# Kernel tuning notes

Hardware: AMD Instinct MI355X
Metric: run time of the kernel (lower is better)

## Reference

```python
import jax, jax.numpy as jnp
import numpy as np

EPS = 1e-5

def _bn_eval(x, gamma, beta, mu, var):
    # channelwise BN (eval mode) on [B,C,N,K]
    inv = gamma / jnp.sqrt(var + EPS)
    return x * inv[None, :, None, None] + (beta - mu * inv)[None, :, None, None]

def _gather_nk(x, idx):
    # x: [B,C,N], idx: [B,N,K] -> [B,C,N,K]
    return jnp.take_along_axis(x[:, :, None, :], idx[:, None, :, :], axis=3)

def setup_inputs() -> dict:
    key = jax.random.key(0)
    ks = jax.random.split(key, 20)
    B, N, K, C = 2, 16384, 16, 128
    s = 0.05
    inp = {
        'coord': jax.random.normal(ks[0], (B, N, 3), jnp.float32),
        'feature_spa': jax.random.normal(ks[1], (B, C, N), jnp.float32),
        'feature_spe': jax.random.normal(ks[2], (B, C, N), jnp.float32),
        'neighbor_indices': jax.random.randint(ks[3], (B, N, K), 0, N),
        'wq': jax.random.normal(ks[4], (C, C), jnp.float32) * s,
        'wk': jax.random.normal(ks[5], (C, C), jnp.float32) * s,
        'wv_w': jax.random.normal(ks[6], (C, C), jnp.float32) * s,
        'wv_b': jax.random.normal(ks[7], (C,), jnp.float32) * s,
        'pos_w1': jax.random.normal(ks[8], (3, 3), jnp.float32) * 0.3,
        'pos_b1': jax.random.normal(ks[9], (3,), jnp.float32) * 0.1,
        'pos_g': jnp.ones((3,), jnp.float32),
        'pos_beta': jnp.zeros((3,), jnp.float32),
        'pos_mu': jnp.zeros((3,), jnp.float32),
        'pos_var': jnp.ones((3,), jnp.float32),
        'pos_w2': jax.random.normal(ks[10], (1, 3), jnp.float32) * 0.3,
        'pos_b2': jax.random.normal(ks[11], (1,), jnp.float32) * 0.1,
        'sc_w1': jax.random.normal(ks[12], (2, 2), jnp.float32) * 0.3,
        'sc_b1': jax.random.normal(ks[13], (2,), jnp.float32) * 0.1,
        'sc_g': jnp.ones((2,), jnp.float32),
        'sc_beta': jnp.zeros((2,), jnp.float32),
        'sc_mu': jnp.zeros((2,), jnp.float32),
        'sc_var': jnp.ones((2,), jnp.float32),
        'sc_w2': jax.random.normal(ks[14], (1, 2), jnp.float32) * 0.3,
        'sc_b2': jax.random.normal(ks[15], (1,), jnp.float32) * 0.1,
    }
    return inp

def reference(coord, feature_spa, feature_spe, neighbor_indices,
              wq, wk, wv_w, wv_b,
              pos_w1, pos_b1, pos_g, pos_beta, pos_mu, pos_var, pos_w2, pos_b2,
              sc_w1, sc_b1, sc_g, sc_beta, sc_mu, sc_var, sc_w2, sc_b2):
    C = feature_spa.shape[1]
    coord_t = jnp.transpose(coord, (0, 2, 1))                      # [B,3,N]
    Q = jnp.einsum('oc,bcn->bon', wq, feature_spa)                 # [B,C,N]
    Kf = jnp.einsum('oc,bcn->bon', wk, feature_spe)
    V = jnp.einsum('oc,bcn->bon', wv_w, feature_spe) + wv_b[None, :, None]
    # positional branch
    neighbor_coord = _gather_nk(coord_t, neighbor_indices)         # [B,3,N,K]
    coord_diff = neighbor_coord - coord_t[:, :, :, None]
    g = jnp.exp(-2.0 * coord_diff ** 2)                            # [B,3,N,K]
    h = jnp.einsum('oc,bcnk->bonk', pos_w1, g) + pos_b1[None, :, None, None]
    h = jax.nn.relu(_bn_eval(h, pos_g, pos_beta, pos_mu, pos_var))
    scores_coord = jnp.einsum('oc,bcnk->bonk', pos_w2, h) + pos_b2[None, :, None, None]  # [B,1,N,K]
    # feature branch
    Kg = _gather_nk(Kf, neighbor_indices)                          # [B,C,N,K]
    Vg = _gather_nk(V, neighbor_indices)                           # [B,C,N,K]
    scores_feat = jnp.einsum('bcn,bcnk->bnk', Q, Kg) / np.sqrt(C)  # [B,N,K]
    scores = jnp.concatenate([scores_coord, scores_feat[:, None]], axis=1)  # [B,2,N,K]
    s = jnp.einsum('oc,bcnk->bonk', sc_w1, scores) + sc_b1[None, :, None, None]
    s = jax.nn.relu(_bn_eval(s, sc_g, sc_beta, sc_mu, sc_var))
    s = jnp.einsum('oc,bcnk->bonk', sc_w2, s) + sc_b2[None, :, None, None]  # [B,1,N,K]
    attn = jax.nn.softmax(s, axis=-1)                              # [B,1,N,K]
    fusion_feat = jnp.sum(attn * Vg, axis=-1)                      # [B,C,N]
    return fusion_feat
```

## Files before the change

### kernel.cpp

```cpp
#include <hip/hip_runtime.h>
#include <cstdint>
#include <cstddef>

#define B_ 2
#define N_ 16384
#define K_ 16
#define C_ 128

typedef __attribute__((ext_vector_type(8))) short  bf16x8;
typedef __attribute__((ext_vector_type(4))) float  f32x4;

__device__ __forceinline__ float bfu_lo(uint32_t w) { return __uint_as_float(w << 16); }
__device__ __forceinline__ float bfu_hi(uint32_t w) { return __uint_as_float(w & 0xffff0000u); }

__device__ __forceinline__ ushort f32_to_bf16_rne(float x) {
    uint32_t u = __float_as_uint(x);
    u += 0x7FFFu + ((u >> 16) & 1u);
    return (ushort)(u >> 16);
}

__device__ __forceinline__ int xswz(int n, int c) {
    return n * 128 + ((((c >> 3) ^ (n & 7)) << 3) | (c & 7));
}

__global__ __launch_bounds__(256) void qkv_gemm(
    const float* __restrict__ spa, const float* __restrict__ spe,
    const float* __restrict__ wq, const float* __restrict__ wk,
    const float* __restrict__ wv, const float* __restrict__ wvb,
    ushort* __restrict__ Qt16, ushort* __restrict__ Kt16, ushort* __restrict__ Vt16)
{
    const int nt    = blockIdx.x * 64;
    const int b     = blockIdx.y;
    const int which = blockIdx.z;
    const float* X = (which == 0) ? spa : spe;
    const float* W = (which == 0) ? wq : (which == 1 ? wk : wv);
    ushort* Out    = (which == 0) ? Qt16 : (which == 1 ? Kt16 : Vt16);

    __shared__ ushort xs[64 * 128];

    const int t    = threadIdx.x;
    const int w    = t >> 6;
    const int lane = t & 63;
    const int l15  = lane & 15;
    const int l4   = lane >> 4;
    const int ow   = (w & 1) * 64;
    const int nw   = (w >> 1) * 32;

    {
        const int c  = t >> 1;
        const int nh = (t & 1) * 32;
        const float* xrow = X + ((size_t)b * C_ + c) * N_ + nt + nh;
        #pragma unroll
        for (int q = 0; q < 8; ++q) {
            float4 v = ((const float4*)xrow)[q];
            const int n = nh + q * 4;
            xs[xswz(n + 0, c)] = f32_to_bf16_rne(v.x);
            xs[xswz(n + 1, c)] = f32_to_bf16_rne(v.y);
            xs[xswz(n + 2, c)] = f32_to_bf16_rne(v.z);
            xs[xswz(n + 3, c)] = f32_to_bf16_rne(v.w);
        }
    }
    __syncthreads();

    f32x4 acc[4][2];
    #pragma unroll
    for (int of = 0; of < 4; ++of)
        #pragma unroll
        for (int nf = 0; nf < 2; ++nf)
            acc[of][nf] = (f32x4){0.f, 0.f, 0.f, 0.f};

    #pragma unroll
    for (int kc = 0; kc < 4; ++kc) {
        const int cb = kc * 32 + l4 * 8;
        bf16x8 afr[4];
        #pragma unroll
        for (int of = 0; of < 4; ++of) {
            const int row = ow + of * 16 + l15;
            const float* wp = W + (size_t)row * C_ + cb;
            float4 wa = *(const float4*)wp;
            float4 wb = *(const float4*)(wp + 4);
            afr[of][0] = (short)f32_to_bf16_rne(wa.x);
            afr[of][1] = (short)f32_to_bf16_rne(wa.y);
            afr[of][2] = (short)f32_to_bf16_rne(wa.z);
            afr[of][3] = (short)f32_to_bf16_rne(wa.w);
            afr[of][4] = (short)f32_to_bf16_rne(wb.x);
            afr[of][5] = (short)f32_to_bf16_rne(wb.y);
            afr[of][6] = (short)f32_to_bf16_rne(wb.z);
            afr[of][7] = (short)f32_to_bf16_rne(wb.w);
        }
        bf16x8 bfr[2];
        #pragma unroll
        for (int nf = 0; nf < 2; ++nf) {
            const int n = nw + nf * 16 + l15;
            bfr[nf] = *(__shared__ bf16x8*)&xs[xswz(n, kc * 32 + l4 * 8)];
        }
        #pragma unroll
        for (int of = 0; of < 4; ++of)
            #pragma unroll
            for (int nf = 0; nf < 2; ++nf)
                acc[of][nf] = __builtin_amdgcn_mfma_f32_16x16x32_bf16(
                    afr[of], bfr[nf], acc[of][nf], 0, 0, 0);
    }

    #pragma unroll
    for (int of = 0; of < 4; ++of) {
        const int o0r = ow + of * 16 + l4 * 4;
        float4 bv = make_float4(0.f, 0.f, 0.f, 0.f);
        if (which == 2) bv = *(const float4*)(wvb + o0r);
        #pragma unroll
        for (int nf = 0; nf < 2; ++nf) {
            const int n = nt + nw + nf * 16 + l15;
            uint2 pk;
            pk.x = (uint32_t)f32_to_bf16_rne(acc[of][nf][0] + bv.x)
                 | ((uint32_t)f32_to_bf16_rne(acc[of][nf][1] + bv.y) << 16);
            pk.y = (uint32_t)f32_to_bf16_rne(acc[of][nf][2] + bv.z)
                 | ((uint32_t)f32_to_bf16_rne(acc[of][nf][3] + bv.w) << 16);
            *(uint2*)(Out + ((size_t)b * N_ + n) * C_ + o0r) = pk;
        }
    }
}

__global__ __launch_bounds__(256) void attn_fuse(
    const float* __restrict__ coord, const int* __restrict__ nbr,
    const ushort* __restrict__ Qt16, const ushort* __restrict__ Kt16,
    const ushort* __restrict__ Vt16,
    const float* __restrict__ pw1, const float* __restrict__ pb1,
    const float* __restrict__ pg,  const float* __restrict__ pbeta,
    const float* __restrict__ pmu, const float* __restrict__ pvar,
    const float* __restrict__ pw2, const float* __restrict__ pb2,
    const float* __restrict__ sw1, const float* __restrict__ sb1,
    const float* __restrict__ sg,  const float* __restrict__ sbeta,
    const float* __restrict__ smu, const float* __restrict__ svar,
    const float* __restrict__ sw2, const float* __restrict__ sb2,
    float* __restrict__ out)
{
    const int bid  = blockIdx.x;
    const int b    = bid >> 10;
    const int n0   = (bid & 1023) << 4;
    const int t    = threadIdx.x;
    const int w    = t >> 6;
    const int lane = t & 63;
    const int g    = lane >> 2;
    const int sub  = lane & 3;

    __shared__ float qs[16][132];
    __shared__ int   idx_s[16][16];
    __shared__ float cs[16][3];
    __shared__ float ot[128][17];

    {
        const int n = t >> 4, c0 = (t & 15) * 8;
        uint4 qw = *(const uint4*)(Qt16 + ((size_t)(b * N_ + n0 + n)) * C_ + c0);
        qs[n][c0 + 0] = bfu_lo(qw.x); qs[n][c0 + 1] = bfu_hi(qw.x);
        qs[n][c0 + 2] = bfu_lo(qw.y); qs[n][c0 + 3] = bfu_hi(qw.y);
        qs[n][c0 + 4] = bfu_lo(qw.z); qs[n][c0 + 5] = bfu_hi(qw.z);
        qs[n][c0 + 6] = bfu_lo(qw.w); qs[n][c0 + 7] = bfu_hi(qw.w);
        idx_s[t >> 4][t & 15] = nbr[((size_t)(b * N_ + n0 + (t >> 4))) * K_ + (t & 15)];
        if (t < 48) cs[t / 3][t % 3] = coord[((size_t)(b * N_ + n0 + t / 3)) * 3 + (t % 3)];
    }
    __syncthreads();

    float pinv[3], pofs[3], w1r[3][3], w2r[3], pb1r[3];
    #pragma unroll
    for (int o = 0; o < 3; ++o) {
        float inv = pg[o] / sqrtf(pvar[o] + 1e-5f);
        pinv[o] = inv;
        pofs[o] = pbeta[o] - pmu[o] * inv;
        pb1r[o] = pb1[o];
        w2r[o]  = pw2[o];
        #pragma unroll
        for (int i2 = 0; i2 < 3; ++i2) w1r[o][i2] = pw1[o * 3 + i2];
    }
    const float pb2v = pb2[0];
    float sinv[2], sofs[2], sb1r[2];
    #pragma unroll
    for (int o = 0; o < 2; ++o) {
        float inv = sg[o] / sqrtf(svar[o] + 1e-5f);
        sinv[o] = inv;
        sofs[o] = sbeta[o] - smu[o] * inv;
        sb1r[o] = sb1[o];
    }
    const float sw1r[4] = {sw1[0], sw1[1], sw1[2], sw1[3]};
    const float sw2r[2] = {sw2[0], sw2[1]};
    const float sb2v = sb2[0];
    const float inv_sqrtC = 0.088388347648318447f;

    #pragma unroll
    for (int i = 0; i < 4; ++i) {
        const int nl = w * 4 + i;
        const int idxg = idx_s[nl][g];

        const uint4* kp = (const uint4*)(Kt16 + ((size_t)(b * N_ + idxg)) * C_ + sub * 32);
        uint4 kw0 = kp[0], kw1 = kp[1], kw2 = kp[2], kw3 = kp[3];
        uint32_t vv[16];
        #pragma unroll
        for (int k = 0; k < 16; ++k) {
            const int vid = idx_s[nl][k];
            vv[k] = ((const uint32_t*)(Vt16 + ((size_t)(b * N_ + vid)) * C_))[lane];
        }
        const float* ncp = coord + ((size_t)(b * N_ + idxg)) * 3;
        const float nc0 = ncp[0], nc1 = ncp[1], nc2 = ncp[2];

        const float* qrow = &qs[nl][sub * 32];
        float acc = 0.f;
        #pragma unroll
        for (int j = 0; j < 4; ++j) {
            float4 qa = *(const float4*)&qrow[j * 8];
            float4 qb = *(const float4*)&qrow[j * 8 + 4];
            uint4  kwj = (j == 0) ? kw0 : (j == 1) ? kw1 : (j == 2) ? kw2 : kw3;
            acc = fmaf(qa.x, bfu_lo(kwj.x), acc);
            acc = fmaf(qa.y, bfu_hi(kwj.x), acc);
            acc = fmaf(qa.z, bfu_lo(kwj.y), acc);
            acc = fmaf(qa.w, bfu_hi(kwj.y), acc);
            acc = fmaf(qb.x, bfu_lo(kwj.z), acc);
            acc = fmaf(qb.y, bfu_hi(kwj.z), acc);
            acc = fmaf(qb.z, bfu_lo(kwj.w), acc);
            acc = fmaf(qb.w, bfu_hi(kwj.w), acc);
        }
        acc += __shfl_xor(acc, 1);
        acc += __shfl_xor(acc, 2);
        const float sfeat = acc * inv_sqrtC;

        float d0 = nc0 - cs[nl][0], d1 = nc1 - cs[nl][1], d2 = nc2 - cs[nl][2];
        float g0 = expf(-2.f * d0 * d0);
        float g1 = expf(-2.f * d1 * d1);
        float g2 = expf(-2.f * d2 * d2);
        float h0 = fmaf(w1r[0][0], g0, fmaf(w1r[0][1], g1, fmaf(w1r[0][2], g2, pb1r[0])));
        float h1 = fmaf(w1r[1][0], g0, fmaf(w1r[1][1], g1, fmaf(w1r[1][2], g2, pb1r[1])));
        float h2 = fmaf(w1r[2][0], g0, fmaf(w1r[2][1], g1, fmaf(w1r[2][2], g2, pb1r[2])));
        h0 = fmaxf(fmaf(h0, pinv[0], pofs[0]), 0.f);
        h1 = fmaxf(fmaf(h1, pinv[1], pofs[1]), 0.f);
        h2 = fmaxf(fmaf(h2, pinv[2], pofs[2]), 0.f);
        const float scoord = fmaf(w2r[0], h0, fmaf(w2r[1], h1, fmaf(w2r[2], h2, pb2v)));

        float t0 = fmaf(sw1r[0], scoord, fmaf(sw1r[1], sfeat, sb1r[0]));
        t0 = fmaxf(fmaf(t0, sinv[0], sofs[0]), 0.f);
        float t1 = fmaf(sw1r[2], scoord, fmaf(sw1r[3], sfeat, sb1r[1]));
        t1 = fmaxf(fmaf(t1, sinv[1], sofs[1]), 0.f);
        float s = fmaf(sw2r[0], t0, fmaf(sw2r[1], t1, sb2v));

        float m = s;
        m = fmaxf(m, __shfl_xor(m, 4));
        m = fmaxf(m, __shfl_xor(m, 8));
        m = fmaxf(m, __shfl_xor(m, 16));
        m = fmaxf(m, __shfl_xor(m, 32));
        float e = expf(s - m);
        float den = e;
        den += __shfl_xor(den, 4);
        den += __shfl_xor(den, 8);
        den += __shfl_xor(den, 16);
        den += __shfl_xor(den, 32);
        const float attn = e / den;

        float a0 = 0.f, a1 = 0.f;
        #pragma unroll
        for (int k = 0; k < 16; ++k) {
            const float ak = __shfl(attn, k << 2);
            a0 = fmaf(ak, bfu_lo(vv[k]), a0);
            a1 = fmaf(ak, bfu_hi(vv[k]), a1);
        }
        ot[2 * lane][nl]     = a0;
        ot[2 * lane + 1][nl] = a1;
    }
    __syncthreads();

    {
        const int col = t & 15;
        const int r0  = (t >> 4) * 8;
        #pragma unroll
        for (int r = 0; r < 8; ++r)
            out[((size_t)(b * C_ + r0 + r)) * N_ + n0 + col] = ot[r0 + r][col];
    }
}

extern "C" void kernel_launch(void* const* d_in, const int* in_sizes, int n_in,
                              void* d_out, int out_size, void* d_ws, size_t ws_size,
                              hipStream_t stream) {
    const float* coord = (const float*)d_in[0];
    const float* spa   = (const float*)d_in[1];
    const float* spe   = (const float*)d_in[2];
    const int*   nbr   = (const int*)  d_in[3];
    const float* wq    = (const float*)d_in[4];
    const float* wk    = (const float*)d_in[5];
    const float* wv    = (const float*)d_in[6];
    const float* wvb   = (const float*)d_in[7];
    const float* pw1   = (const float*)d_in[8];
    const float* pb1   = (const float*)d_in[9];
    const float* pg    = (const float*)d_in[10];
    const float* pbeta = (const float*)d_in[11];
    const float* pmu   = (const float*)d_in[12];
    const float* pvar  = (const float*)d_in[13];
    const float* pw2   = (const float*)d_in[14];
    const float* pb2   = (const float*)d_in[15];
    const float* sw1   = (const float*)d_in[16];
    const float* sb1   = (const float*)d_in[17];
    const float* sg    = (const float*)d_in[18];
    const float* sbeta = (const float*)d_in[19];
    const float* smu   = (const float*)d_in[20];
    const float* svar  = (const float*)d_in[21];
    const float* sw2   = (const float*)d_in[22];
    const float* sb2   = (const float*)d_in[23];
    float* out = (float*)d_out;

    ushort* Qt16 = (ushort*)d_ws;
    ushort* Kt16 = Qt16 + (size_t)B_ * N_ * C_;
    ushort* Vt16 = Kt16 + (size_t)B_ * N_ * C_;

    qkv_gemm<<<dim3(N_ / 64, B_, 3), 256, 0, stream>>>(
        spa, spe, wq, wk, wv, wvb, Qt16, Kt16, Vt16);

    attn_fuse<<<dim3(B_ * N_ / 16), 256, 0, stream>>>(
        coord, nbr, Qt16, Kt16, Vt16,
        pw1, pb1, pg, pbeta, pmu, pvar, pw2, pb2,
        sw1, sb1, sg, sbeta, smu, svar, sw2, sb2,
        out);
}
```

Measured before the change: 192.3 us.

## Pre-convert QKV weights to bf16 and stage them in LDS with larger GEMM tiles

Adds a small kernel that converts the three weight matrices to bf16 once per call. The QKV GEMM then loads the whole bf16 weight matrix into swizzled shared memory instead of reading and converting fp32 weights from global memory in every block. The N tile grows from 64 to 128 with 512 threads, which halves the number of blocks and raises reuse. In exchange it adds a kernel launch, needs 64KB of LDS per block (which may limit occupancy), and uses extra workspace for the converted weights.

```diff
diff --git a/kernel.cpp b/kernel.cpp
--- a/kernel.cpp
+++ b/kernel.cpp
@@ -18,42 +18,72 @@
     u += 0x7FFFu + ((u >> 16) & 1u);
     return (ushort)(u >> 16);
 }
-
-__device__ __forceinline__ int xswz(int n, int c) {
-    return n * 128 + ((((c >> 3) ^ (n & 7)) << 3) | (c & 7));
-}
-
-__global__ __launch_bounds__(256) void qkv_gemm(
+__device__ __forceinline__ uint32_t pack_bf16x2(float lo, float hi) {
+    return (uint32_t)f32_to_bf16_rne(lo) | ((uint32_t)f32_to_bf16_rne(hi) << 16);
+}
+
+__device__ __forceinline__ int xswz(int row, int c) {
+    return row * 128 + ((((c >> 3) ^ (row & 7)) << 3) | (c & 7));
+}
+
+__global__ __launch_bounds__(256) void w_cvt(
+    const float* __restrict__ wq, const float* __restrict__ wk,
+    const float* __restrict__ wv, ushort* __restrict__ W16all)
+{
+    const float* src = (blockIdx.y == 0) ? wq : (blockIdx.y == 1 ? wk : wv);
+    ushort* dst = W16all + (size_t)blockIdx.y * (C_ * C_);
+    const int i = (blockIdx.x * 256 + threadIdx.x) * 8;
+    float4 a = *(const float4*)(src + i);
+    float4 b4 = *(const float4*)(src + i + 4);
+    uint4 pk;
+    pk.x = pack_bf16x2(a.x, a.y);
+    pk.y = pack_bf16x2(a.z, a.w);
+    pk.z = pack_bf16x2(b4.x, b4.y);
+    pk.w = pack_bf16x2(b4.z, b4.w);
+    *(uint4*)(dst + i) = pk;
+}
+
+__global__ __launch_bounds__(512) void qkv_gemm(
     const float* __restrict__ spa, const float* __restrict__ spe,
-    const float* __restrict__ wq, const float* __restrict__ wk,
-    const float* __restrict__ wv, const float* __restrict__ wvb,
+    const ushort* __restrict__ W16all, const float* __restrict__ wvb,
     ushort* __restrict__ Qt16, ushort* __restrict__ Kt16, ushort* __restrict__ Vt16)
 {
-    const int nt    = blockIdx.x * 64;
+    const int nt    = blockIdx.x * 128;
     const int b     = blockIdx.y;
     const int which = blockIdx.z;
-    const float* X = (which == 0) ? spa : spe;
-    const float* W = (which == 0) ? wq : (which == 1 ? wk : wv);
-    ushort* Out    = (which == 0) ? Qt16 : (which == 1 ? Kt16 : Vt16);
-
-    __shared__ ushort xs[64 * 128];
+    const float*  X   = (which == 0) ? spa : spe;
+    const ushort* W16 = W16all + (size_t)which * (C_ * C_);
+    ushort* Out       = (which == 0) ? Qt16 : (which == 1 ? Kt16 : Vt16);
+
+    __shared__ ushort xs[128 * 128];
+    __shared__ ushort ws[128 * 128];
 
     const int t    = threadIdx.x;
     const int w    = t >> 6;
     const int lane = t & 63;
     const int l15  = lane & 15;
     const int l4   = lane >> 4;
-    const int ow   = (w & 1) * 64;
-    const int nw   = (w >> 1) * 32;
+    const int ow   = (w & 3) * 32;
+    const int nw   = (w >> 2) * 64;
 
     {
-        const int c  = t >> 1;
-        const int nh = (t & 1) * 32;
-        const float* xrow = X + ((size_t)b * C_ + c) * N_ + nt + nh;
+        const int r  = t >> 2;
+        const int c0 = (t & 3) * 32;
+        const uint4* src = (const uint4*)(W16 + r * C_ + c0);
+        #pragma unroll
+        for (int q = 0; q < 4; ++q) {
+            uint4 v = src[q];
+            *(uint4*)&ws[xswz(r, c0 + q * 8)] = v;
+        }
+    }
+    {
+        const int c  = t >> 2;
+        const int nq = (t & 3) * 32;
+        const float* xrow = X + ((size_t)b * C_ + c) * N_ + nt + nq;
         #pragma unroll
         for (int q = 0; q < 8; ++q) {
             float4 v = ((const float4*)xrow)[q];
-            const int n = nh + q * 4;
+            const int n = nq + q * 4;
             xs[xswz(n + 0, c)] = f32_to_bf16_rne(v.x);
             xs[xswz(n + 1, c)] = f32_to_bf16_rne(v.y);
             xs[xswz(n + 2, c)] = f32_to_bf16_rne(v.z);
@@ -62,59 +92,43 @@
     }
     __syncthreads();
 
-    f32x4 acc[4][2];
-    #pragma unroll
-    for (int of = 0; of < 4; ++of)
-        #pragma unroll
-        for (int nf = 0; nf < 2; ++nf)
+    f32x4 acc[2][4];
+    #pragma unroll
+    for (int of = 0; of < 2; ++of)
+        #pragma unroll
+        for (int nf = 0; nf < 4; ++nf)
             acc[of][nf] = (f32x4){0.f, 0.f, 0.f, 0.f};
 
     #pragma unroll
     for (int kc = 0; kc < 4; ++kc) {
         const int cb = kc * 32 + l4 * 8;
-        bf16x8 afr[4];
-        #pragma unroll
-        for (int of = 0; of < 4; ++of) {
-            const int row = ow + of * 16 + l15;
-            const float* wp = W + (size_t)row * C_ + cb;
-            float4 wa = *(const float4*)wp;
-            float4 wb = *(const float4*)(wp + 4);
-            afr[of][0] = (short)f32_to_bf16_rne(wa.x);
-            afr[of][1] = (short)f32_to_bf16_rne(wa.y);
-            afr[of][2] = (short)f32_to_bf16_rne(wa.z);
-            afr[of][3] = (short)f32_to_bf16_rne(wa.w);
-            afr[of][4] = (short)f32_to_bf16_rne(wb.x);
-            afr[of][5] = (short)f32_to_bf16_rne(wb.y);
-            afr[of][6] = (short)f32_to_bf16_rne(wb.z);
-            afr[of][7] = (short)f32_to_bf16_rne(wb.w);
-        }
-        bf16x8 bfr[2];
-        #pragma unroll
-        for (int nf = 0; nf < 2; ++nf) {
-            const int n = nw + nf * 16 + l15;
-            bfr[nf] = *(__shared__ bf16x8*)&xs[xswz(n, kc * 32 + l4 * 8)];
-        }
-        #pragma unroll
-        for (int of = 0; of < 4; ++of)
+        bf16x8 afr[2];
+        #pragma unroll
+        for (int of = 0; of < 2; ++of)
+            afr[of] = *(__shared__ bf16x8*)&ws[xswz(ow + of * 16 + l15, cb)];
+        bf16x8 bfr[4];
+        #pragma unroll
+        for (int nf = 0; nf < 4; ++nf)
+            bfr[nf] = *(__shared__ bf16x8*)&xs[xswz(nw + nf * 16 + l15, cb)];
+        #pragma unroll
+        for (int of = 0; of < 2; ++of)
             #pragma unroll
-            for (int nf = 0; nf < 2; ++nf)
+            for (int nf = 0; nf < 4; ++nf)
                 acc[of][nf] = __builtin_amdgcn_mfma_f32_16x16x32_bf16(
                     afr[of], bfr[nf], acc[of][nf], 0, 0, 0);
     }
 
     #pragma unroll
-    for (int of = 0; of < 4; ++of) {
+    for (int of = 0; of < 2; ++of) {
         const int o0r = ow + of * 16 + l4 * 4;
         float4 bv = make_float4(0.f, 0.f, 0.f, 0.f);
         if (which == 2) bv = *(const float4*)(wvb + o0r);
         #pragma unroll
-        for (int nf = 0; nf < 2; ++nf) {
+        for (int nf = 0; nf < 4; ++nf) {
             const int n = nt + nw + nf * 16 + l15;
             uint2 pk;
-            pk.x = (uint32_t)f32_to_bf16_rne(acc[of][nf][0] + bv.x)
-                 | ((uint32_t)f32_to_bf16_rne(acc[of][nf][1] + bv.y) << 16);
-            pk.y = (uint32_t)f32_to_bf16_rne(acc[of][nf][2] + bv.z)
-                 | ((uint32_t)f32_to_bf16_rne(acc[of][nf][3] + bv.w) << 16);
+            pk.x = pack_bf16x2(acc[of][nf][0] + bv.x, acc[of][nf][1] + bv.y);
+            pk.y = pack_bf16x2(acc[of][nf][2] + bv.z, acc[of][nf][3] + bv.w);
             *(uint2*)(Out + ((size_t)b * N_ + n) * C_ + o0r) = pk;
         }
     }
@@ -302,12 +316,15 @@
     const float* sb2   = (const float*)d_in[23];
     float* out = (float*)d_out;
 
-    ushort* Qt16 = (ushort*)d_ws;
-    ushort* Kt16 = Qt16 + (size_t)B_ * N_ * C_;
-    ushort* Vt16 = Kt16 + (size_t)B_ * N_ * C_;
-
-    qkv_gemm<<<dim3(N_ / 64, B_, 3), 256, 0, stream>>>(
-        spa, spe, wq, wk, wv, wvb, Qt16, Kt16, Vt16);
+    ushort* Qt16  = (ushort*)d_ws;
+    ushort* Kt16  = Qt16 + (size_t)B_ * N_ * C_;
+    ushort* Vt16  = Kt16 + (size_t)B_ * N_ * C_;
+    ushort* W16all = Vt16 + (size_t)B_ * N_ * C_;
+
+    w_cvt<<<dim3(8, 3), 256, 0, stream>>>(wq, wk, wv, W16all);
+
+    qkv_gemm<<<dim3(N_ / 128, B_, 3), 512, 0, stream>>>(
+        spa, spe, W16all, wvb, Qt16, Kt16, Vt16);
 
     attn_fuse<<<dim3(B_ * N_ / 16), 256, 0, stream>>>(
         coord, nbr, Qt16, Kt16, Vt16,
```

Result: faster. 173.5 us (-9.7%).
